# Performance work log

Hardware: AMD Instinct MI355X
Metric: run time of the kernel (lower is better)

The kernel has to match this reference:

```python
import jax, jax.numpy as jnp
import numpy as np

B, F, D = 4096, 39, 16          # batch, num_field, embedding_size
V = 1000000                     # num_feat (vocab)
H1, H2 = 128, 128               # cin_layer_sizes
INPUT_DIM = F * D               # 624
FC_DIM = H1 // 2 + H2           # 192 (split_half)
DEEP = [400, 400]
BN_EPS = 1e-5


def setup_inputs() -> dict:
    key = jax.random.key(0)
    ks = jax.random.split(key, 16)
    xav = lambda k, shp: jax.random.normal(k, shp, jnp.float32) * np.sqrt(2.0 / (shp[0] + shp[-1]))
    return {
        "feat_index": jax.random.randint(ks[0], (B, F), 0, V),
        "feat_value": jax.random.uniform(ks[1], (B, F), jnp.float32),
        "emb_table": xav(ks[2], (V, D)),
        "linear_w": xav(ks[3], (INPUT_DIM, 1)),
        "linear_b": jnp.zeros((1,), jnp.float32),
        "conv_w1": xav(ks[4], (H1, F, F)),          # (out, h_prev, m) == conv1d 1x1 weight reshaped
        "conv_b1": jnp.zeros((H1,), jnp.float32),
        "conv_w2": xav(ks[5], (H2, H1 // 2, F)),
        "conv_b2": jnp.zeros((H2,), jnp.float32),
        "deep_w1": xav(ks[6], (INPUT_DIM, DEEP[0])),
        "deep_b1": jnp.zeros((DEEP[0],), jnp.float32),
        "bn_g1": jnp.ones((DEEP[0],), jnp.float32),
        "bn_b1": jnp.zeros((DEEP[0],), jnp.float32),
        "deep_w2": xav(ks[7], (DEEP[0], DEEP[1])),
        "deep_b2": jnp.zeros((DEEP[1],), jnp.float32),
        "bn_g2": jnp.ones((DEEP[1],), jnp.float32),
        "bn_b2": jnpp if False else jnp.zeros((DEEP[1],), jnp.float32),
        "out_w": xav(ks[8], (1 + FC_DIM + DEEP[1], 1)),
        "out_b": jnp.zeros((1,), jnp.float32),
    }


def _bn(x, g, b):
    # torch BatchNorm1d in training mode: biased batch variance
    m = x.mean(axis=0)
    v = x.var(axis=0)
    return g * (x - m) * jax.lax.rsqrt(v + BN_EPS) + b


def reference(feat_index, feat_value, emb_table, linear_w, linear_b,
              conv_w1, conv_b1, conv_w2, conv_b2,
              deep_w1, deep_b1, bn_g1, bn_b1,
              deep_w2, deep_b2, bn_g2, bn_b2,
              out_w, out_b):
    e = emb_table[feat_index]                      # [B, F, D]
    flat = e.reshape(e.shape[0], -1)               # [B, F*D]
    linear_part = flat @ linear_w + linear_b       # [B, 1]

    # CIN: fused outer-product + 1x1 conv (x_k[b,o,d] = sum_{h,m} W[o,h,m] x_prev[b,h,d] x0[b,m,d])
    x0 = e
    h1 = jax.nn.relu(jnp.einsum('bhd,bmd,ohm->bod', x0, x0, conv_w1) + conv_b1[None, :, None])
    nxt, hi1 = jnp.split(h1, 2, axis=1)            # split_half
    h2 = jax.nn.relu(jnp.einsum('bhd,bmd,ohm->bod', nxt, x0, conv_w2) + conv_b2[None, :, None])
    res = jnp.concatenate([hi1, h2], axis=1).sum(axis=2)   # [B, FC_DIM]

    # Deep tower (dropout off / deterministic)
    y = jax.nn.relu(_bn(flat @ deep_w1 + deep_b1, bn_g1, bn_b1))
    y = jax.nn.relu(_bn(y @ deep_w2 + deep_b2, bn_g2, bn_b2))

    cat = jnp.concatenate([linear_part, res, y], axis=1)   # [B, 593]
    return cat @ out_w + out_b
```

## Files before the change

### kernel.cpp

```cpp
#include <hip/hip_runtime.h>

#define BATCH   4096
#define NF      39
#define ED      16
#define IN_DIM  624
#define DW      400
#define BN_EPS  1e-5f
#define KTOT    2496
#define NKSG    78
#define AK1     640
#define NKS1    20
#define NKS2    13

typedef __attribute__((ext_vector_type(8))) short short8;
typedef __attribute__((ext_vector_type(4))) float f32x4;
typedef unsigned short u16;

__device__ inline unsigned pack2_trunc(float a, float b) {
  return (__float_as_uint(a) >> 16) | (__float_as_uint(b) & 0xffff0000u);
}
__device__ inline unsigned bf16_rne(float f) {
  unsigned u = __float_as_uint(f);
  u += 0x7fff + ((u >> 16) & 1);
  return u >> 16;
}
__device__ inline float bf2f(u16 v) { return __uint_as_float((unsigned)v << 16); }

__global__ __launch_bounds__(256) void k_gather(const int* __restrict__ idx,
    const float* __restrict__ emb, const float* __restrict__ lw,
    const float* __restrict__ lb, u16* __restrict__ flatb,
    float* __restrict__ lp) {
  int b = blockIdx.x, t = threadIdx.x;
  __shared__ int si[NF];
  if (t < NF) si[t] = idx[b * NF + t];
  __syncthreads();
  float acc = 0.f;
#pragma unroll
  for (int i = 0; i < 3; i++) {
    int e = t + i * 256;
    if (e < IN_DIM) {
      float v = emb[(size_t)si[e >> 4] * ED + (e & 15)];
      flatb[(size_t)b * AK1 + e] = (u16)bf16_rne(v);
      acc = fmaf(v, lw[e], acc);
    } else if (e < AK1) {
      flatb[(size_t)b * AK1 + e] = 0;
    }
  }
#pragma unroll
  for (int k = 1; k < 64; k <<= 1) acc += __shfl_xor(acc, k);
  __shared__ float r4[4];
  if ((t & 63) == 0) r4[t >> 6] = acc;
  __syncthreads();
  if (t == 0) lp[b] = r4[0] + r4[1] + r4[2] + r4[3] + lb[0];
}

__global__ __launch_bounds__(256) void k_prep(const float* __restrict__ w1,
    const float* __restrict__ w2, const float* __restrict__ dw1,
    const float* __restrict__ dw2, u16* __restrict__ wp1, u16* __restrict__ wp2,
    u16* __restrict__ wpd1, u16* __restrict__ wpd2, float* __restrict__ gstat) {
  const int CIN_E = NKSG * 128 * 32;
  const int D1_E  = NKS1 * 400 * 32;
  const int D2_E  = NKS2 * 400 * 32;
  int e = blockIdx.x * 256 + threadIdx.x;
  if (e < CIN_E) {
    int ksg = e >> 12, r = e & 4095, n = r >> 5, kk = r & 31;
    int k = ksg * 32 + kk, h = k & 63, m = k >> 6;
    float v1 = (h < NF) ? w1[(size_t)n * (NF * NF) + h * NF + m] : 0.f;
    float v2 = w2[(size_t)n * (64 * NF) + h * NF + m];
    wp1[e] = (u16)bf16_rne(v1);
    wp2[e] = (u16)bf16_rne(v2);
  } else if (e < CIN_E + D1_E) {
    int e2 = e - CIN_E;
    int ksg = e2 / 12800, r = e2 - ksg * 12800, col = r >> 5, kk = r & 31;
    int k = ksg * 32 + kk;
    wpd1[e2] = (k < IN_DIM) ? (u16)bf16_rne(dw1[(size_t)k * DW + col]) : 0;
  } else if (e < CIN_E + D1_E + D2_E) {
    int e2 = e - CIN_E - D1_E;
    int ksg = e2 / 12800, r = e2 - ksg * 12800, col = r >> 5, kk = r & 31;
    int k = ksg * 32 + kk;
    wpd2[e2] = (k < DW) ? (u16)bf16_rne(dw2[(size_t)k * DW + col]) : 0;
  } else if (e < CIN_E + D1_E + D2_E + 1600) {
    gstat[e - CIN_E - D1_E - D2_E] = 0.f;
  }
}

template <bool LAY2>
__global__ __launch_bounds__(256, 2) void k_cin_mfma(
    const u16* __restrict__ flatb, const u16* __restrict__ nxtg,
    const u16* __restrict__ wp, const float* __restrict__ bias,
    u16* __restrict__ nxt_out, float* __restrict__ res) {
  int t = threadIdx.x;
  int w = t >> 6, lane = t & 63;
  int nl = lane & 15, q = lane >> 4;
  int d = nl;
  int b0 = blockIdx.x * 16 + w * 4;
  int c0 = blockIdx.y * 64;

  unsigned nxr[4][2][4];
  if (LAY2) {
#pragma unroll
    for (int si = 0; si < 4; si++)
#pragma unroll
      for (int ks = 0; ks < 2; ks++) {
        uint4 v = *(const uint4*)(nxtg +
            (((size_t)(b0 + si) * 16 + d) * 64 + ks * 32 + q * 8));
        nxr[si][ks][0] = v.x; nxr[si][ks][1] = v.y;
        nxr[si][ks][2] = v.z; nxr[si][ks][3] = v.w;
      }
  } else {
#pragma unroll
    for (int si = 0; si < 4; si++)
#pragma unroll
      for (int ks = 0; ks < 2; ks++)
#pragma unroll
        for (int w4 = 0; w4 < 4; w4++) {
          int h0 = ks * 32 + q * 8 + 2 * w4;
          int h1 = h0 + 1;
          unsigned u0 = (h0 < NF) ? flatb[(size_t)(b0 + si) * AK1 + h0 * 16 + d] : 0;
          unsigned u1 = (h1 < NF) ? flatb[(size_t)(b0 + si) * AK1 + h1 * 16 + d] : 0;
          nxr[si][ks][w4] = u0 | (u1 << 16);
        }
  }

  f32x4 acc[4][4];
#pragma unroll
  for (int si = 0; si < 4; si++)
#pragma unroll
    for (int nt = 0; nt < 4; nt++) acc[si][nt] = (f32x4){0.f, 0.f, 0.f, 0.f};

  const u16* wbase = wp + (size_t)(c0 + nl) * 32 + q * 8;
  short8 bfr[2][4];
#pragma unroll
  for (int nt = 0; nt < 4; nt++)
    bfr[0][nt] = *(const short8*)(wbase + nt * 512);

  float xv[4], xvn[4];
#pragma unroll
  for (int si = 0; si < 4; si++)
    xv[si] = bf2f(flatb[(size_t)(b0 + si) * AK1 + d]);

  for (int m = 0; m < NF; m++) {
    if (m + 1 < NF) {
#pragma unroll
      for (int si = 0; si < 4; si++)
        xvn[si] = bf2f(flatb[(size_t)(b0 + si) * AK1 + (m + 1) * 16 + d]);
    }
#pragma unroll
    for (int ks = 0; ks < 2; ks++) {
      int ksg = m * 2 + ks;
      int cur = ksg & 1, nxt = cur ^ 1;
      if (ksg + 1 < NKSG) {
        const u16* wb = wbase + (size_t)(ksg + 1) * 4096;
#pragma unroll
        for (int nt = 0; nt < 4; nt++)
          bfr[nxt][nt] = *(const short8*)(wb + nt * 512);
      }
      short8 afr[4];
#pragma unroll
      for (int si = 0; si < 4; si++) {
        union { unsigned u[4]; short8 s; } a;
#pragma unroll
        for (int w4 = 0; w4 < 4; w4++) {
          unsigned u = nxr[si][ks][w4];
          float lo = __uint_as_float(u << 16) * xv[si];
          float hi = __uint_as_float(u & 0xffff0000u) * xv[si];
          a.u[w4] = pack2_trunc(lo, hi);
        }
        afr[si] = a.s;
      }
#pragma unroll
      for (int nt = 0; nt < 4; nt++)
#pragma unroll
        for (int si = 0; si < 4; si++)
          acc[si][nt] = __builtin_amdgcn_mfma_f32_16x16x32_bf16(
              afr[si], bfr[cur][nt], acc[si][nt], 0, 0, 0);
    }
#pragma unroll
    for (int si = 0; si < 4; si++) xv[si] = xvn[si];
  }

#pragma unroll
  for (int si = 0; si < 4; si++) {
    int b = b0 + si;
#pragma unroll
    for (int nt = 0; nt < 4; nt++) {
      int o = c0 + nt * 16 + nl;
      float bi = bias[o];
      if (!LAY2 && c0 == 0) {
#pragma unroll
        for (int r = 0; r < 4; r++) {
          float v = fmaxf(acc[si][nt][r] + bi, 0.f);
          nxt_out[((size_t)b * 16 + q * 4 + r) * 64 + o] = (u16)bf16_rne(v);
        }
      } else {
        float s = 0.f;
#pragma unroll
        for (int r = 0; r < 4; r++) s += fmaxf(acc[si][nt][r] + bi, 0.f);
        s += __shfl_xor(s, 16);
        s += __shfl_xor(s, 32);
        if (q == 0) {
          int ri = LAY2 ? (64 + o) : (o - 64);
          res[(size_t)b * 192 + ri] = s;
        }
      }
    }
  }
}

template <bool BN_A, int NKS, int KREAL>
__global__ __launch_bounds__(256) void k_gemm_mfma(
    const u16* __restrict__ Abf, const float* __restrict__ Af32,
    const u16* __restrict__ wp, const float* __restrict__ bias,
    const float* __restrict__ bnS, const float* __restrict__ bnSh,
    float* __restrict__ C, float* __restrict__ gs, float* __restrict__ gs2) {
  __shared__ float ls[160];
  int t = threadIdx.x;
  if (t < 160) ls[t] = 0.f;
  __syncthreads();
  int w = t >> 6, lane = t & 63;
  int nl = lane & 15, q = lane >> 4;
  int row = blockIdx.x * 64 + w * 16 + nl;
  int c0 = blockIdx.y * 80;
  f32x4 acc[5];
#pragma unroll
  for (int nt = 0; nt < 5; nt++) acc[nt] = (f32x4){0.f, 0.f, 0.f, 0.f};

  for (int ksg = 0; ksg < NKS; ksg++) {
    int kb = ksg * 32 + q * 8;
    short8 afr;
    if (!BN_A) {
      afr = *(const short8*)(Abf + (size_t)row * (NKS * 32) + kb);
    } else {
      if (kb + 8 <= KREAL) {
        const float* ap = Af32 + (size_t)row * KREAL + kb;
        float4 f0 = *(const float4*)ap;
        float4 f1 = *(const float4*)(ap + 4);
        union { unsigned u[4]; short8 s; } a;
        float v0 = fmaxf(fmaf(f0.x, bnS[kb + 0], bnSh[kb + 0]), 0.f);
        float v1 = fmaxf(fmaf(f0.y, bnS[kb + 1], bnSh[kb + 1]), 0.f);
        float v2 = fmaxf(fmaf(f0.z, bnS[kb + 2], bnSh[kb + 2]), 0.f);
        float v3 = fmaxf(fmaf(f0.w, bnS[kb + 3], bnSh[kb + 3]), 0.f);
        float v4 = fmaxf(fmaf(f1.x, bnS[kb + 4], bnSh[kb + 4]), 0.f);
        float v5 = fmaxf(fmaf(f1.y, bnS[kb + 5], bnSh[kb + 5]), 0.f);
        float v6 = fmaxf(fmaf(f1.z, bnS[kb + 6], bnSh[kb + 6]), 0.f);
        float v7 = fmaxf(fmaf(f1.w, bnS[kb + 7], bnSh[kb + 7]), 0.f);
        a.u[0] = bf16_rne(v0) | (bf16_rne(v1) << 16);
        a.u[1] = bf16_rne(v2) | (bf16_rne(v3) << 16);
        a.u[2] = bf16_rne(v4) | (bf16_rne(v5) << 16);
        a.u[3] = bf16_rne(v6) | (bf16_rne(v7) << 16);
        afr = a.s;
      } else {
        union { unsigned u[4]; short8 s; } a;
        a.u[0] = a.u[1] = a.u[2] = a.u[3] = 0;
        afr = a.s;
      }
    }
    const u16* wb = wp + (size_t)ksg * (400 * 32) + (size_t)(c0 + nl) * 32 + q * 8;
#pragma unroll
    for (int nt = 0; nt < 5; nt++) {
      short8 bfr = *(const short8*)(wb + nt * 512);
      acc[nt] = __builtin_amdgcn_mfma_f32_16x16x32_bf16(afr, bfr, acc[nt], 0, 0, 0);
    }
  }

  int rbase = blockIdx.x * 64 + w * 16 + q * 4;
#pragma unroll
  for (int nt = 0; nt < 5; nt++) {
    int col = c0 + nt * 16 + nl;
    float bi = bias[col];
    float s = 0.f, s2 = 0.f;
#pragma unroll
    for (int r = 0; r < 4; r++) {
      float v = acc[nt][r] + bi;
      C[(size_t)(rbase + r) * DW + col] = v;
      s += v; s2 = fmaf(v, v, s2);
    }
    s += __shfl_xor(s, 16); s2 += __shfl_xor(s2, 16);
    s += __shfl_xor(s, 32); s2 += __shfl_xor(s2, 32);
    if (q == 0) {
      atomicAdd(&ls[nt * 16 + nl], s);
      atomicAdd(&ls[80 + nt * 16 + nl], s2);
    }
  }
  __syncthreads();
  if (t < 80)       atomicAdd(&gs[c0 + t], ls[t]);
  else if (t < 160) atomicAdd(&gs2[c0 + t - 80], ls[t]);
}

__global__ __launch_bounds__(256) void k_bnfin(const float* __restrict__ gs,
    const float* __restrict__ gs2, const float* __restrict__ g,
    const float* __restrict__ bt, float* __restrict__ sc, float* __restrict__ sh) {
  int c = blockIdx.x * 256 + threadIdx.x;
  if (c >= DW) return;
  float m = gs[c] * (1.f / BATCH);
  float var = gs2[c] * (1.f / BATCH) - m * m;
  float scl = g[c] * rsqrtf(var + BN_EPS);
  sc[c] = scl;
  sh[c] = bt[c] - m * scl;
}

__global__ __launch_bounds__(256) void k_final(const float* __restrict__ lp,
    const float* __restrict__ res, const float* __restrict__ y2,
    const float* __restrict__ sc2, const float* __restrict__ sh2,
    const float* __restrict__ ow, const float* __restrict__ ob,
    float* __restrict__ out) {
  int t = threadIdx.x;
  int lane = t & 63, w = t >> 6;
  int b = blockIdx.x * 4 + w;
  float acc = 0.f;
  for (int j = lane; j < 593; j += 64) {
    float v;
    if (j == 0)       v = lp[b];
    else if (j < 193) v = res[(size_t)b * 192 + (j - 1)];
    else {
      int c = j - 193;
      v = fmaxf(fmaf(y2[(size_t)b * DW + c], sc2[c], sh2[c]), 0.f);
    }
    acc = fmaf(v, ow[j], acc);
  }
#pragma unroll
  for (int k = 1; k < 64; k <<= 1) acc += __shfl_xor(acc, k);
  if (lane == 0) out[b] = acc + ob[0];
}

extern "C" void kernel_launch(void* const* d_in, const int* in_sizes, int n_in,
                              void* d_out, int out_size, void* d_ws, size_t ws_size,
                              hipStream_t stream) {
  const int*   feat_index = (const int*)d_in[0];
  const float* emb = (const float*)d_in[2];
  const float* lw  = (const float*)d_in[3];
  const float* lb  = (const float*)d_in[4];
  const float* w1  = (const float*)d_in[5];
  const float* b1  = (const float*)d_in[6];
  const float* w2  = (const float*)d_in[7];
  const float* b2  = (const float*)d_in[8];
  const float* dw1 = (const float*)d_in[9];
  const float* db1 = (const float*)d_in[10];
  const float* g1  = (const float*)d_in[11];
  const float* bb1 = (const float*)d_in[12];
  const float* dw2 = (const float*)d_in[13];
  const float* db2 = (const float*)d_in[14];
  const float* g2  = (const float*)d_in[15];
  const float* bb2 = (const float*)d_in[16];
  const float* ow  = (const float*)d_in[17];
  const float* ob  = (const float*)d_in[18];

  float* ws   = (float*)d_ws;
  u16*  flatb = (u16*)ws;
  float* y1   = ws + 1310720;
  float* res  = ws + 2949120;
  float* lp   = ws + 3735552;
  float* bn1s = ws + 3739648;
  float* bn1b = bn1s + 400;
  float* bn2s = bn1b + 400;
  float* bn2b = bn2s + 400;
  float* gA   = ws + 3741248;
  float* gA2  = gA + 400;
  float* gB   = gA2 + 400;
  float* gB2  = gB + 400;
  u16*  nxtg  = (u16*)(ws + 3742848);
  float* y2   = ws + 3742848;
  u16*  wp1   = (u16*)(ws + 5840000);
  u16*  wp2   = (u16*)(ws + 5999744);
  u16*  wpd1  = (u16*)(ws + 6159488);
  u16*  wpd2  = (u16*)(ws + 6287488);
  float* out  = (float*)d_out;

  const int PREP_E = NKSG * 128 * 32 + NKS1 * 400 * 32 + NKS2 * 400 * 32 + 1600;

  k_gather<<<BATCH, 256, 0, stream>>>(feat_index, emb, lw, lb, flatb, lp);
  k_prep<<<(PREP_E + 255) / 256, 256, 0, stream>>>(w1, w2, dw1, dw2, wp1, wp2,
                                                   wpd1, wpd2, gA);
  k_cin_mfma<false><<<dim3(BATCH / 16, 2), 256, 0, stream>>>(
      flatb, nullptr, wp1, b1, nxtg, res);
  k_cin_mfma<true><<<dim3(BATCH / 16, 2), 256, 0, stream>>>(
      flatb, nxtg, wp2, b2, nullptr, res);
  k_gemm_mfma<false, NKS1, IN_DIM><<<dim3(BATCH / 64, 5), 256, 0, stream>>>(
      flatb, nullptr, wpd1, db1, nullptr, nullptr, y1, gA, gA2);
  k_bnfin<<<2, 256, 0, stream>>>(gA, gA2, g1, bb1, bn1s, bn1b);
  k_gemm_mfma<true, NKS2, DW><<<dim3(BATCH / 64, 5), 256, 0, stream>>>(
      nullptr, y1, wpd2, db2, bn1s, bn1b, y2, gB, gB2);
  k_bnfin<<<2, 256, 0, stream>>>(gB, gB2, g2, bb2, bn2s, bn2b);
  k_final<<<BATCH / 4, 256, 0, stream>>>(lp, res, y2, bn2s, bn2b, ow, ob, out);
}
```

Measured before the change: 280.4 us.

## Merge gather/prep, split CIN K across wave pairs, narrow GEMM tiles, fold BN finalize

Merges the gather and weight-prep kernels into one launch. Splits the CIN field loop across two waves per batch group, with the partial sums reduced through LDS, and raises occupancy to 4 blocks per CU. The deep GEMMs now use 16-column tiles with 25 column blocks and double-buffered raw loads. The BN finalize kernels are removed and their scale/shift is computed inside each consumer block. The goal is fewer launches and more parallelism, at the cost of redundant BN stat math per block, reduced reuse of A loads in the GEMMs, and an extra barrier plus LDS traffic in CIN.

```diff
diff --git a/kernel.cpp b/kernel.cpp
--- a/kernel.cpp
+++ b/kernel.cpp
@@ -26,75 +26,84 @@
 }
 __device__ inline float bf2f(u16 v) { return __uint_as_float((unsigned)v << 16); }
 
-__global__ __launch_bounds__(256) void k_gather(const int* __restrict__ idx,
+#define CIN_E (NKSG * 128 * 32)
+#define D1_E  (NKS1 * 400 * 32)
+#define D2_E  (NKS2 * 400 * 32)
+#define PREP_E (CIN_E + D1_E + D2_E + 1600)
+#define PREP_B ((PREP_E + 255) / 256)
+
+__global__ __launch_bounds__(256) void k_gp(const int* __restrict__ idx,
     const float* __restrict__ emb, const float* __restrict__ lw,
-    const float* __restrict__ lb, u16* __restrict__ flatb,
-    float* __restrict__ lp) {
-  int b = blockIdx.x, t = threadIdx.x;
-  __shared__ int si[NF];
-  if (t < NF) si[t] = idx[b * NF + t];
-  __syncthreads();
-  float acc = 0.f;
-#pragma unroll
-  for (int i = 0; i < 3; i++) {
-    int e = t + i * 256;
-    if (e < IN_DIM) {
-      float v = emb[(size_t)si[e >> 4] * ED + (e & 15)];
-      flatb[(size_t)b * AK1 + e] = (u16)bf16_rne(v);
-      acc = fmaf(v, lw[e], acc);
-    } else if (e < AK1) {
-      flatb[(size_t)b * AK1 + e] = 0;
-    }
-  }
-#pragma unroll
-  for (int k = 1; k < 64; k <<= 1) acc += __shfl_xor(acc, k);
-  __shared__ float r4[4];
-  if ((t & 63) == 0) r4[t >> 6] = acc;
-  __syncthreads();
-  if (t == 0) lp[b] = r4[0] + r4[1] + r4[2] + r4[3] + lb[0];
-}
-
-__global__ __launch_bounds__(256) void k_prep(const float* __restrict__ w1,
+    const float* __restrict__ lb, const float* __restrict__ w1,
     const float* __restrict__ w2, const float* __restrict__ dw1,
-    const float* __restrict__ dw2, u16* __restrict__ wp1, u16* __restrict__ wp2,
+    const float* __restrict__ dw2, u16* __restrict__ flatb,
+    float* __restrict__ lp, u16* __restrict__ wp1, u16* __restrict__ wp2,
     u16* __restrict__ wpd1, u16* __restrict__ wpd2, float* __restrict__ gstat) {
-  const int CIN_E = NKSG * 128 * 32;
-  const int D1_E  = NKS1 * 400 * 32;
-  const int D2_E  = NKS2 * 400 * 32;
-  int e = blockIdx.x * 256 + threadIdx.x;
-  if (e < CIN_E) {
-    int ksg = e >> 12, r = e & 4095, n = r >> 5, kk = r & 31;
-    int k = ksg * 32 + kk, h = k & 63, m = k >> 6;
-    float v1 = (h < NF) ? w1[(size_t)n * (NF * NF) + h * NF + m] : 0.f;
-    float v2 = w2[(size_t)n * (64 * NF) + h * NF + m];
-    wp1[e] = (u16)bf16_rne(v1);
-    wp2[e] = (u16)bf16_rne(v2);
-  } else if (e < CIN_E + D1_E) {
-    int e2 = e - CIN_E;
-    int ksg = e2 / 12800, r = e2 - ksg * 12800, col = r >> 5, kk = r & 31;
-    int k = ksg * 32 + kk;
-    wpd1[e2] = (k < IN_DIM) ? (u16)bf16_rne(dw1[(size_t)k * DW + col]) : 0;
-  } else if (e < CIN_E + D1_E + D2_E) {
-    int e2 = e - CIN_E - D1_E;
-    int ksg = e2 / 12800, r = e2 - ksg * 12800, col = r >> 5, kk = r & 31;
-    int k = ksg * 32 + kk;
-    wpd2[e2] = (k < DW) ? (u16)bf16_rne(dw2[(size_t)k * DW + col]) : 0;
-  } else if (e < CIN_E + D1_E + D2_E + 1600) {
-    gstat[e - CIN_E - D1_E - D2_E] = 0.f;
+  int t = threadIdx.x;
+  if (blockIdx.x < BATCH) {
+    int b = blockIdx.x;
+    __shared__ int si[NF];
+    __shared__ float r4[4];
+    if (t < NF) si[t] = idx[b * NF + t];
+    __syncthreads();
+    float acc = 0.f;
+#pragma unroll
+    for (int i = 0; i < 3; i++) {
+      int e = t + i * 256;
+      if (e < IN_DIM) {
+        float v = emb[(size_t)si[e >> 4] * ED + (e & 15)];
+        flatb[(size_t)b * AK1 + e] = (u16)bf16_rne(v);
+        acc = fmaf(v, lw[e], acc);
+      } else if (e < AK1) {
+        flatb[(size_t)b * AK1 + e] = 0;
+      }
+    }
+#pragma unroll
+    for (int k = 1; k < 64; k <<= 1) acc += __shfl_xor(acc, k);
+    if ((t & 63) == 0) r4[t >> 6] = acc;
+    __syncthreads();
+    if (t == 0) lp[b] = r4[0] + r4[1] + r4[2] + r4[3] + lb[0];
+  } else {
+    int e = (blockIdx.x - BATCH) * 256 + t;
+    if (e < CIN_E) {
+      int ksg = e >> 12, r = e & 4095, n = r >> 5, kk = r & 31;
+      int k = ksg * 32 + kk, h = k & 63, m = k >> 6;
+      float v1 = (h < NF) ? w1[(size_t)n * (NF * NF) + h * NF + m] : 0.f;
+      float v2 = w2[(size_t)n * (64 * NF) + h * NF + m];
+      wp1[e] = (u16)bf16_rne(v1);
+      wp2[e] = (u16)bf16_rne(v2);
+    } else if (e < CIN_E + D1_E) {
+      int e2 = e - CIN_E;
+      int ksg = e2 / 12800, r = e2 - ksg * 12800, col = r >> 5, kk = r & 31;
+      int k = ksg * 32 + kk;
+      wpd1[e2] = (k < IN_DIM) ? (u16)bf16_rne(dw1[(size_t)k * DW + col]) : 0;
+    } else if (e < CIN_E + D1_E + D2_E) {
+      int e2 = e - CIN_E - D1_E;
+      int ksg = e2 / 12800, r = e2 - ksg * 12800, col = r >> 5, kk = r & 31;
+      int k = ksg * 32 + kk;
+      wpd2[e2] = (k < DW) ? (u16)bf16_rne(dw2[(size_t)k * DW + col]) : 0;
+    } else if (e < PREP_E) {
+      gstat[e - CIN_E - D1_E - D2_E] = 0.f;
+    }
   }
 }
 
 template <bool LAY2>
-__global__ __launch_bounds__(256, 2) void k_cin_mfma(
+__global__ __launch_bounds__(256, 4) void k_cin_mfma(
     const u16* __restrict__ flatb, const u16* __restrict__ nxtg,
     const u16* __restrict__ wp, const float* __restrict__ bias,
     u16* __restrict__ nxt_out, float* __restrict__ res) {
+  __shared__ f32x4 lds4[2 * 16 * 64];
   int t = threadIdx.x;
   int w = t >> 6, lane = t & 63;
+  int pair = w >> 1, half = w & 1;
   int nl = lane & 15, q = lane >> 4;
   int d = nl;
-  int b0 = blockIdx.x * 16 + w * 4;
+  int b0 = blockIdx.x * 8 + pair * 4;
   int c0 = blockIdx.y * 64;
+  int M0 = half ? 20 : 0;
+  int M1 = half ? NF : 20;
+  int NLOC = (M1 - M0) * 2;
 
   unsigned nxr[4][2][4];
   if (LAY2) {
@@ -128,7 +137,7 @@
 #pragma unroll
     for (int nt = 0; nt < 4; nt++) acc[si][nt] = (f32x4){0.f, 0.f, 0.f, 0.f};
 
-  const u16* wbase = wp + (size_t)(c0 + nl) * 32 + q * 8;
+  const u16* wbase = wp + (size_t)(c0 + nl) * 32 + q * 8 + (size_t)M0 * 2 * 4096;
   short8 bfr[2][4];
 #pragma unroll
   for (int nt = 0; nt < 4; nt++)
@@ -137,31 +146,32 @@
   float xv[4], xvn[4];
 #pragma unroll
   for (int si = 0; si < 4; si++)
-    xv[si] = bf2f(flatb[(size_t)(b0 + si) * AK1 + d]);
-
-  for (int m = 0; m < NF; m++) {
-    if (m + 1 < NF) {
+    xv[si] = bf2f(flatb[(size_t)(b0 + si) * AK1 + M0 * 16 + d]);
+
+  for (int m = M0; m < M1; m++) {
+    if (m + 1 < M1) {
 #pragma unroll
       for (int si = 0; si < 4; si++)
         xvn[si] = bf2f(flatb[(size_t)(b0 + si) * AK1 + (m + 1) * 16 + d]);
     }
 #pragma unroll
     for (int ks = 0; ks < 2; ks++) {
-      int ksg = m * 2 + ks;
-      int cur = ksg & 1, nxt = cur ^ 1;
-      if (ksg + 1 < NKSG) {
-        const u16* wb = wbase + (size_t)(ksg + 1) * 4096;
+      int local = (m - M0) * 2 + ks;
+      int cur = local & 1, nx = cur ^ 1;
+      if (local + 1 < NLOC) {
+        const u16* wb = wbase + (size_t)(local + 1) * 4096;
 #pragma unroll
         for (int nt = 0; nt < 4; nt++)
-          bfr[nxt][nt] = *(const short8*)(wb + nt * 512);
-      }
+          bfr[nx][nt] = *(const short8*)(wb + nt * 512);
+      }
+      int mks = (m & 0) + ks;
       short8 afr[4];
 #pragma unroll
       for (int si = 0; si < 4; si++) {
         union { unsigned u[4]; short8 s; } a;
 #pragma unroll
         for (int w4 = 0; w4 < 4; w4++) {
-          unsigned u = nxr[si][ks][w4];
+          unsigned u = nxr[si][mks][w4];
           float lo = __uint_as_float(u << 16) * xv[si];
           float hi = __uint_as_float(u & 0xffff0000u) * xv[si];
           a.u[w4] = pack2_trunc(lo, hi);
@@ -178,6 +188,24 @@
 #pragma unroll
     for (int si = 0; si < 4; si++) xv[si] = xvn[si];
   }
+
+  if (half) {
+#pragma unroll
+    for (int si = 0; si < 4; si++)
+#pragma unroll
+      for (int nt = 0; nt < 4; nt++)
+        lds4[(pair * 16 + si * 4 + nt) * 64 + lane] = acc[si][nt];
+  }
+  __syncthreads();
+  if (half) return;
+#pragma unroll
+  for (int si = 0; si < 4; si++)
+#pragma unroll
+    for (int nt = 0; nt < 4; nt++) {
+      f32x4 p = lds4[(pair * 16 + si * 4 + nt) * 64 + lane];
+      acc[si][nt][0] += p[0]; acc[si][nt][1] += p[1];
+      acc[si][nt][2] += p[2]; acc[si][nt][3] += p[3];
+    }
 
 #pragma unroll
   for (int si = 0; si < 4; si++) {
@@ -207,104 +235,121 @@
   }
 }
 
-template <bool BN_A, int NKS, int KREAL>
+template <bool BN_A, int NKS, int KREAL, int AK>
 __global__ __launch_bounds__(256) void k_gemm_mfma(
     const u16* __restrict__ Abf, const float* __restrict__ Af32,
     const u16* __restrict__ wp, const float* __restrict__ bias,
-    const float* __restrict__ bnS, const float* __restrict__ bnSh,
+    const float* __restrict__ gsIn, const float* __restrict__ gs2In,
+    const float* __restrict__ bng, const float* __restrict__ bnb,
     float* __restrict__ C, float* __restrict__ gs, float* __restrict__ gs2) {
-  __shared__ float ls[160];
+  __shared__ float lsS[NKS * 32], lsH[NKS * 32];
+  __shared__ float lred[32];
   int t = threadIdx.x;
-  if (t < 160) ls[t] = 0.f;
+  if (BN_A) {
+    for (int c = t; c < NKS * 32; c += 256) {
+      float sc = 0.f, sh = 0.f;
+      if (c < DW) {
+        float m = gsIn[c] * (1.f / BATCH);
+        float var = gs2In[c] * (1.f / BATCH) - m * m;
+        sc = bng[c] * rsqrtf(var + BN_EPS);
+        sh = bnb[c] - m * sc;
+      }
+      lsS[c] = sc; lsH[c] = sh;
+    }
+  }
+  if (t < 32) lred[t] = 0.f;
   __syncthreads();
+
   int w = t >> 6, lane = t & 63;
   int nl = lane & 15, q = lane >> 4;
   int row = blockIdx.x * 64 + w * 16 + nl;
-  int c0 = blockIdx.y * 80;
-  f32x4 acc[5];
-#pragma unroll
-  for (int nt = 0; nt < 5; nt++) acc[nt] = (f32x4){0.f, 0.f, 0.f, 0.f};
-
-  for (int ksg = 0; ksg < NKS; ksg++) {
+  int c0 = blockIdx.y * 16;
+  f32x4 acc = (f32x4){0.f, 0.f, 0.f, 0.f};
+
+  short8 araw[2]; f32x4 fraw0[2], fraw1[2]; short8 braw[2];
+  auto loadA_raw = [&](int ksg, int buf) {
     int kb = ksg * 32 + q * 8;
-    short8 afr;
     if (!BN_A) {
-      afr = *(const short8*)(Abf + (size_t)row * (NKS * 32) + kb);
+      araw[buf] = *(const short8*)(Abf + (size_t)row * AK + kb);
     } else {
       if (kb + 8 <= KREAL) {
-        const float* ap = Af32 + (size_t)row * KREAL + kb;
-        float4 f0 = *(const float4*)ap;
-        float4 f1 = *(const float4*)(ap + 4);
-        union { unsigned u[4]; short8 s; } a;
-        float v0 = fmaxf(fmaf(f0.x, bnS[kb + 0], bnSh[kb + 0]), 0.f);
-        float v1 = fmaxf(fmaf(f0.y, bnS[kb + 1], bnSh[kb + 1]), 0.f);
-        float v2 = fmaxf(fmaf(f0.z, bnS[kb + 2], bnSh[kb + 2]), 0.f);
-        float v3 = fmaxf(fmaf(f0.w, bnS[kb + 3], bnSh[kb + 3]), 0.f);
-        float v4 = fmaxf(fmaf(f1.x, bnS[kb + 4], bnSh[kb + 4]), 0.f);
-        float v5 = fmaxf(fmaf(f1.y, bnS[kb + 5], bnSh[kb + 5]), 0.f);
-        float v6 = fmaxf(fmaf(f1.z, bnS[kb + 6], bnSh[kb + 6]), 0.f);
-        float v7 = fmaxf(fmaf(f1.w, bnS[kb + 7], bnSh[kb + 7]), 0.f);
-        a.u[0] = bf16_rne(v0) | (bf16_rne(v1) << 16);
-        a.u[1] = bf16_rne(v2) | (bf16_rne(v3) << 16);
-        a.u[2] = bf16_rne(v4) | (bf16_rne(v5) << 16);
-        a.u[3] = bf16_rne(v6) | (bf16_rne(v7) << 16);
-        afr = a.s;
+        fraw0[buf] = *(const f32x4*)(Af32 + (size_t)row * KREAL + kb);
+        fraw1[buf] = *(const f32x4*)(Af32 + (size_t)row * KREAL + kb + 4);
       } else {
-        union { unsigned u[4]; short8 s; } a;
-        a.u[0] = a.u[1] = a.u[2] = a.u[3] = 0;
-        afr = a.s;
-      }
-    }
-    const u16* wb = wp + (size_t)ksg * (400 * 32) + (size_t)(c0 + nl) * 32 + q * 8;
-#pragma unroll
-    for (int nt = 0; nt < 5; nt++) {
-      short8 bfr = *(const short8*)(wb + nt * 512);
-      acc[nt] = __builtin_amdgcn_mfma_f32_16x16x32_bf16(afr, bfr, acc[nt], 0, 0, 0);
-    }
+        fraw0[buf] = (f32x4){0.f,0.f,0.f,0.f};
+        fraw1[buf] = (f32x4){0.f,0.f,0.f,0.f};
+      }
+    }
+    braw[buf] = *(const short8*)(wp + (size_t)ksg * (400 * 32) +
+                                 (size_t)(c0 + nl) * 32 + q * 8);
+  };
+  auto cookA = [&](int ksg, int buf) -> short8 {
+    if (!BN_A) return araw[buf];
+    int kb = ksg * 32 + q * 8;
+    f32x4 s0 = *(const f32x4*)&lsS[kb], h0 = *(const f32x4*)&lsH[kb];
+    f32x4 s1 = *(const f32x4*)&lsS[kb + 4], h1 = *(const f32x4*)&lsH[kb + 4];
+    union { unsigned u[4]; short8 s; } a;
+    float v0 = fmaxf(fmaf(fraw0[buf][0], s0[0], h0[0]), 0.f);
+    float v1 = fmaxf(fmaf(fraw0[buf][1], s0[1], h0[1]), 0.f);
+    float v2 = fmaxf(fmaf(fraw0[buf][2], s0[2], h0[2]), 0.f);
+    float v3 = fmaxf(fmaf(fraw0[buf][3], s0[3], h0[3]), 0.f);
+    float v4 = fmaxf(fmaf(fraw1[buf][0], s1[0], h1[0]), 0.f);
+    float v5 = fmaxf(fmaf(fraw1[buf][1], s1[1], h1[1]), 0.f);
+    float v6 = fmaxf(fmaf(fraw1[buf][2], s1[2], h1[2]), 0.f);
+    float v7 = fmaxf(fmaf(fraw1[buf][3], s1[3], h1[3]), 0.f);
+    a.u[0] = bf16_rne(v0) | (bf16_rne(v1) << 16);
+    a.u[1] = bf16_rne(v2) | (bf16_rne(v3) << 16);
+    a.u[2] = bf16_rne(v4) | (bf16_rne(v5) << 16);
+    a.u[3] = bf16_rne(v6) | (bf16_rne(v7) << 16);
+    return a.s;
+  };
+
+  loadA_raw(0, 0);
+#pragma unroll 4
+  for (int ksg = 0; ksg < NKS; ksg++) {
+    int cur = ksg & 1;
+    if (ksg + 1 < NKS) loadA_raw(ksg + 1, cur ^ 1);
+    short8 afr = cookA(ksg, cur);
+    acc = __builtin_amdgcn_mfma_f32_16x16x32_bf16(afr, braw[cur], acc, 0, 0, 0);
   }
 
   int rbase = blockIdx.x * 64 + w * 16 + q * 4;
-#pragma unroll
-  for (int nt = 0; nt < 5; nt++) {
-    int col = c0 + nt * 16 + nl;
-    float bi = bias[col];
-    float s = 0.f, s2 = 0.f;
-#pragma unroll
-    for (int r = 0; r < 4; r++) {
-      float v = acc[nt][r] + bi;
-      C[(size_t)(rbase + r) * DW + col] = v;
-      s += v; s2 = fmaf(v, v, s2);
-    }
-    s += __shfl_xor(s, 16); s2 += __shfl_xor(s2, 16);
-    s += __shfl_xor(s, 32); s2 += __shfl_xor(s2, 32);
-    if (q == 0) {
-      atomicAdd(&ls[nt * 16 + nl], s);
-      atomicAdd(&ls[80 + nt * 16 + nl], s2);
-    }
+  int col = c0 + nl;
+  float bi = bias[col];
+  float s = 0.f, s2 = 0.f;
+#pragma unroll
+  for (int r = 0; r < 4; r++) {
+    float v = acc[r] + bi;
+    C[(size_t)(rbase + r) * DW + col] = v;
+    s += v; s2 = fmaf(v, v, s2);
+  }
+  s += __shfl_xor(s, 16); s2 += __shfl_xor(s2, 16);
+  s += __shfl_xor(s, 32); s2 += __shfl_xor(s2, 32);
+  if (q == 0) {
+    atomicAdd(&lred[nl], s);
+    atomicAdd(&lred[16 + nl], s2);
   }
   __syncthreads();
-  if (t < 80)       atomicAdd(&gs[c0 + t], ls[t]);
-  else if (t < 160) atomicAdd(&gs2[c0 + t - 80], ls[t]);
-}
-
-__global__ __launch_bounds__(256) void k_bnfin(const float* __restrict__ gs,
-    const float* __restrict__ gs2, const float* __restrict__ g,
-    const float* __restrict__ bt, float* __restrict__ sc, float* __restrict__ sh) {
-  int c = blockIdx.x * 256 + threadIdx.x;
-  if (c >= DW) return;
-  float m = gs[c] * (1.f / BATCH);
-  float var = gs2[c] * (1.f / BATCH) - m * m;
-  float scl = g[c] * rsqrtf(var + BN_EPS);
-  sc[c] = scl;
-  sh[c] = bt[c] - m * scl;
+  if (t < 16)       atomicAdd(&gs[c0 + t], lred[t]);
+  else if (t < 32)  atomicAdd(&gs2[c0 + t - 16], lred[t]);
 }
 
 __global__ __launch_bounds__(256) void k_final(const float* __restrict__ lp,
     const float* __restrict__ res, const float* __restrict__ y2,
-    const float* __restrict__ sc2, const float* __restrict__ sh2,
+    const float* __restrict__ gB, const float* __restrict__ gB2,
+    const float* __restrict__ g2, const float* __restrict__ bb2,
     const float* __restrict__ ow, const float* __restrict__ ob,
     float* __restrict__ out) {
+  __shared__ float lsS[DW], lsH[DW];
   int t = threadIdx.x;
+  for (int c = t; c < DW; c += 256) {
+    float m = gB[c] * (1.f / BATCH);
+    float var = gB2[c] * (1.f / BATCH) - m * m;
+    float sc = g2[c] * rsqrtf(var + BN_EPS);
+    lsS[c] = sc;
+    lsH[c] = bb2[c] - m * sc;
+  }
+  __syncthreads();
   int lane = t & 63, w = t >> 6;
   int b = blockIdx.x * 4 + w;
   float acc = 0.f;
@@ -314,7 +359,7 @@
     else if (j < 193) v = res[(size_t)b * 192 + (j - 1)];
     else {
       int c = j - 193;
-      v = fmaxf(fmaf(y2[(size_t)b * DW + c], sc2[c], sh2[c]), 0.f);
+      v = fmaxf(fmaf(y2[(size_t)b * DW + c], lsS[c], lsH[c]), 0.f);
     }
     acc = fmaf(v, ow[j], acc);
   }
@@ -350,10 +395,6 @@
   float* y1   = ws + 1310720;
   float* res  = ws + 2949120;
   float* lp   = ws + 3735552;
-  float* bn1s = ws + 3739648;
-  float* bn1b = bn1s + 400;
-  float* bn2s = bn1b + 400;
-  float* bn2b = bn2s + 400;
   float* gA   = ws + 3741248;
   float* gA2  = gA + 400;
   float* gB   = gA2 + 400;
@@ -366,20 +407,15 @@
   u16*  wpd2  = (u16*)(ws + 6287488);
   float* out  = (float*)d_out;
 
-  const int PREP_E = NKSG * 128 * 32 + NKS1 * 400 * 32 + NKS2 * 400 * 32 + 1600;
-
-  k_gather<<<BATCH, 256, 0, stream>>>(feat_index, emb, lw, lb, flatb, lp);
-  k_prep<<<(PREP_E + 255) / 256, 256, 0, stream>>>(w1, w2, dw1, dw2, wp1, wp2,
-                                                   wpd1, wpd2, gA);
-  k_cin_mfma<false><<<dim3(BATCH / 16, 2), 256, 0, stream>>>(
+  k_gp<<<BATCH + PREP_B, 256, 0, stream>>>(feat_index, emb, lw, lb, w1, w2,
+      dw1, dw2, flatb, lp, wp1, wp2, wpd1, wpd2, gA);
+  k_cin_mfma<false><<<dim3(BATCH / 8, 2), 256, 0, stream>>>(
       flatb, nullptr, wp1, b1, nxtg, res);
-  k_cin_mfma<true><<<dim3(BATCH / 16, 2), 256, 0, stream>>>(
+  k_cin_mfma<true><<<dim3(BATCH / 8, 2), 256, 0, stream>>>(
       flatb, nxtg, wp2, b2, nullptr, res);
-  k_gemm_mfma<false, NKS1, IN_DIM><<<dim3(BATCH / 64, 5), 256, 0, stream>>>(
-      flatb, nullptr, wpd1, db1, nullptr, nullptr, y1, gA, gA2);
-  k_bnfin<<<2, 256, 0, stream>>>(gA, gA2, g1, bb1, bn1s, bn1b);
-  k_gemm_mfma<true, NKS2, DW><<<dim3(BATCH / 64, 5), 256, 0, stream>>>(
-      nullptr, y1, wpd2, db2, bn1s, bn1b, y2, gB, gB2);
-  k_bnfin<<<2, 256, 0, stream>>>(gB, gB2, g2, bb2, bn2s, bn2b);
-  k_final<<<BATCH / 4, 256, 0, stream>>>(lp, res, y2, bn2s, bn2b, ow, ob, out);
-}
+  k_gemm_mfma<false, NKS1, IN_DIM, AK1><<<dim3(BATCH / 64, 25), 256, 0, stream>>>(
+      flatb, nullptr, wpd1, db1, nullptr, nullptr, nullptr, nullptr, y1, gA, gA2);
+  k_gemm_mfma<true, NKS2, DW, 0><<<dim3(BATCH / 64, 25), 256, 0, stream>>>(
+      nullptr, y1, wpd2, db2, gA, gA2, g1, bb1, y2, gB, gB2);
+  k_final<<<BATCH / 4, 256, 0, stream>>>(lp, res, y2, gB, gB2, g2, bb2, ow, ob, out);
+}
```

Measured after the change: 657.1 us. 134% more time.
